# Kernel optimization log

Measured on AMD Instinct MI355X. Metric: run time of the kernel, lower is better.

The kernel has to match this reference:

```python
import math
import jax, jax.numpy as jnp
import numpy as np
from jax import lax

B, CIN, COUT, K, SDIM, H, W = 8, 64, 64, 3, 512, 256, 256
EPS = 1e-8

def setup_inputs() -> dict:
    key = jax.random.key(0)
    k1, k2, k3, k4 = jax.random.split(key, 4)
    return {
        "input": jax.random.normal(k1, (B, CIN, H, W), dtype=jnp.float32),
        "style": jax.random.normal(k2, (B, SDIM), dtype=jnp.float32),
        "weight": jax.random.normal(k3, (1, COUT, CIN, K, K), dtype=jnp.float32),
        "mod_weight": jax.random.normal(k4, (CIN, SDIM), dtype=jnp.float32),
        "mod_bias": jnp.ones((CIN,), dtype=jnp.float32),
    }

def reference(input, style, weight, mod_weight, mod_bias):
    b, cin, h, w = input.shape
    cout, k = weight.shape[1], weight.shape[3]
    scale = 1.0 / math.sqrt(cin * k * k)          # equalized-lr conv scale
    mod_scale = 1.0 / math.sqrt(mod_weight.shape[1])  # EqualLinear fan-in scale
    # style modulation: (B, Cin)
    s = jnp.einsum('bs,cs->bc', style, mod_weight) * mod_scale + mod_bias
    # modulated per-sample weights: (B, Cout, Cin, K, K)
    wmod = scale * weight * s[:, None, :, None, None]
    # demodulation over (Cin, K, K)
    demod = lax.rsqrt(jnp.sum(wmod * wmod, axis=(2, 3, 4)) + EPS)
    wmod = wmod * demod[:, :, None, None, None]
    # grouped conv with groups = batch
    x = input.reshape(1, b * cin, h, w)
    wg = wmod.reshape(b * cout, cin, k, k)
    pad = k // 2
    out = lax.conv_general_dilated(
        x, wg, window_strides=(1, 1), padding=[(pad, pad), (pad, pad)],
        dimension_numbers=('NCHW', 'OIHW', 'NCHW'), feature_group_count=b)
    return out.reshape(b, cout, h, w)
```

## Files before the change

### kernel.cpp

```cpp
#include <hip/hip_runtime.h>


#define CIN   64
#define COUT  64
#define SDIM  512
#define HW    256

typedef short bf16x8 __attribute__((ext_vector_type(8)));
typedef float f32x4  __attribute__((ext_vector_type(4)));
typedef unsigned short u16;

static __device__ __forceinline__ u16 f2bf(float f) {
    union { float f; unsigned u; } v; v.f = f;
    unsigned r = v.u + 0x7FFF + ((v.u >> 16) & 1);
    return (u16)(r >> 16);
}

__global__ void k_style(const float* __restrict__ style, const float* __restrict__ mw,
                        const float* __restrict__ mb, float* __restrict__ s_out) {
    int b = blockIdx.x;
    int t = threadIdx.x;
    int cin = t & 63, seg = t >> 6;
    const float4* st = (const float4*)(style + (size_t)b * SDIM) + seg * 32;
    const float4* w  = (const float4*)(mw + (size_t)cin * SDIM) + seg * 32;
    float acc = 0.f;
#pragma unroll 8
    for (int i = 0; i < 32; i++) {
        float4 a = st[i], bb = w[i];
        acc += a.x * bb.x + a.y * bb.y + a.z * bb.z + a.w * bb.w;
    }
    __shared__ float red[4][64];
    red[seg][cin] = acc;
    __syncthreads();
    if (seg == 0) {
        float v = red[0][cin] + red[1][cin] + red[2][cin] + red[3][cin];
        s_out[b * CIN + cin] = v * 0.04419417382415922f + mb[cin];
    }
}

__global__ void k_wdemod(const float* __restrict__ weight, const float* __restrict__ s,
                         u16* __restrict__ wA) {
    int bid = blockIdx.x;
    int b = bid >> 6, co = bid & 63;
    int cin = threadIdx.x;
    float sv = s[b * CIN + cin] * (1.0f / 24.0f);
    const float* wp = weight + ((size_t)co * CIN + cin) * 9;
    float w[9]; float sq = 0.f;
#pragma unroll
    for (int k = 0; k < 9; k++) { w[k] = wp[k] * sv; sq += w[k] * w[k]; }
#pragma unroll
    for (int off = 32; off; off >>= 1) sq += __shfl_xor(sq, off, 64);
    float dm = 1.0f / sqrtf(sq + 1e-8f);
    u16* dst = wA + (((size_t)b * COUT + co) * 9) * 64 + cin;
#pragma unroll
    for (int k = 0; k < 9; k++) dst[k * 64] = f2bf(w[k] * dm);
}

__global__ void k_transpose(const float* __restrict__ in, u16* __restrict__ X) {
    int bid = blockIdx.x;
    int wblk = bid & 3, h = (bid >> 2) & 255, b = bid >> 10;
    int w0 = wblk * 64;
    __shared__ u16 lds[64][65];
    int t = threadIdx.x;
    const float* src = in + (size_t)b * CIN * 65536 + (size_t)h * 256 + w0;
    int dw = t & 63, c0 = t >> 6;
#pragma unroll
    for (int i = 0; i < 16; i++) {
        int cin = i * 4 + c0;
        lds[cin][dw] = f2bf(src[(size_t)cin * 65536 + dw]);
    }
    __syncthreads();
    u16* dst = X + (((size_t)b * 256 + h) * 256 + w0) * 64;
#pragma unroll
    for (int i = 0; i < 4; i++) {
        int u = i * 256 + t;
        int dw2 = u >> 4, c4 = (u & 15) * 4;
        ushort4 val;
        val.x = lds[c4 + 0][dw2]; val.y = lds[c4 + 1][dw2];
        val.z = lds[c4 + 2][dw2]; val.w = lds[c4 + 3][dw2];
        *(ushort4*)(dst + (size_t)dw2 * 64 + c4) = val;
    }
}

__global__ __launch_bounds__(256, 2) void k_conv(
        const u16* __restrict__ X, const u16* __restrict__ wA,
        float* __restrict__ out) {
    int bid = blockIdx.x;
    int b = bid >> 8, r = bid & 255;
    int y0 = (r >> 2) << 2;
    int x0 = (r & 3) << 6;
    int wv = threadIdx.x >> 6;
    int l  = threadIdx.x & 63;
    int lr = l & 15, lg = l >> 4;
    int y = y0 + wv;

    f32x4 acc[4][4];
#pragma unroll
    for (int ct = 0; ct < 4; ct++)
#pragma unroll
        for (int xt = 0; xt < 4; xt++) acc[ct][xt] = (f32x4){0.f, 0.f, 0.f, 0.f};

    const u16* Xb  = X  + (size_t)b * 65536 * 64;
    const u16* wAb = wA + (size_t)b * COUT * 9 * 64;

#pragma unroll
    for (int kk = 0; kk < 9; kk++) {
        const int dh = kk / 3, dw = kk % 3;
        int yy = y + dh - 1;
        if (yy < 0 || yy > 255) continue;
        const u16* Xrow = Xb + (size_t)yy * 256 * 64;
#pragma unroll
        for (int half = 0; half < 2; half++) {
            bf16x8 afr[4], bfr[4];
#pragma unroll
            for (int ct = 0; ct < 4; ct++) {
                afr[ct] = *(const bf16x8*)(wAb + (((size_t)(ct * 16 + lr)) * 9 + kk) * 64
                                           + half * 32 + lg * 8);
            }
#pragma unroll
            for (int xt = 0; xt < 4; xt++) {
                int xx = x0 + xt * 16 + lr + dw - 1;
                bf16x8 v = {0, 0, 0, 0, 0, 0, 0, 0};
                if (xx >= 0 && xx < 256)
                    v = *(const bf16x8*)(Xrow + (size_t)xx * 64 + half * 32 + lg * 8);
                bfr[xt] = v;
            }
#pragma unroll
            for (int ct = 0; ct < 4; ct++)
#pragma unroll
                for (int xt = 0; xt < 4; xt++)
                    acc[ct][xt] = __builtin_amdgcn_mfma_f32_16x16x32_bf16(
                        afr[ct], bfr[xt], acc[ct][xt], 0, 0, 0);
        }
    }

    float* ob = out + (size_t)b * COUT * 65536 + (size_t)y * 256 + x0;
#pragma unroll
    for (int ct = 0; ct < 4; ct++)
#pragma unroll
        for (int xt = 0; xt < 4; xt++)
#pragma unroll
            for (int q = 0; q < 4; q++) {
                int cout = ct * 16 + lg * 4 + q;
                ob[(size_t)cout * 65536 + xt * 16 + lr] = acc[ct][xt][q];
            }
}

extern "C" void kernel_launch(void* const* d_in, const int* in_sizes, int n_in,
                              void* d_out, int out_size, void* d_ws, size_t ws_size,
                              hipStream_t stream) {
    const float* input      = (const float*)d_in[0];
    const float* style      = (const float*)d_in[1];
    const float* weight     = (const float*)d_in[2];
    const float* mod_weight = (const float*)d_in[3];
    const float* mod_bias   = (const float*)d_in[4];
    float* out = (float*)d_out;

    char* ws = (char*)d_ws;
    u16*   X  = (u16*)ws;
    u16*   wA = (u16*)(ws + 67108864);
    float* s  = (float*)(ws + 67108864 + 589824);

    k_style    <<<8,    256, 0, stream>>>(style, mod_weight, mod_bias, s);
    k_wdemod   <<<512,  64,  0, stream>>>(weight, s, wA);
    k_transpose<<<8192, 256, 0, stream>>>(input, X);
    k_conv     <<<2048, 256, 0, stream>>>(X, wA, out);
}
```

Before: 373.7 us.

## Fuse input transpose into conv via LDS halo tile and stage output stores

Removes the separate transpose kernel and its 64 MB bf16 intermediate. The conv kernel now loads an fp32 6x72x64 halo tile straight from the NCHW input, converts it to bf16 into XOR-swizzled LDS, and reads MFMA B fragments from LDS instead of global memory. The epilogue goes through LDS so each cout row is written with coalesced float4 stores, and block indices are swizzled across batches. In exchange, each block reloads halo rows that neighbouring blocks also read, and the kernel uses about 55 KB of LDS, which may limit occupancy.

```diff
diff --git a/kernel.cpp b/kernel.cpp
--- a/kernel.cpp
+++ b/kernel.cpp
@@ -1,19 +1,23 @@
 #include <hip/hip_runtime.h>
+#include <hip/hip_bf16.h>
 
 
 #define CIN   64
 #define COUT  64
 #define SDIM  512
-#define HW    256
 
 typedef short bf16x8 __attribute__((ext_vector_type(8)));
 typedef float f32x4  __attribute__((ext_vector_type(4)));
 typedef unsigned short u16;
+typedef unsigned short us8 __attribute__((ext_vector_type(8)));
 
 static __device__ __forceinline__ u16 f2bf(float f) {
     union { float f; unsigned u; } v; v.f = f;
     unsigned r = v.u + 0x7FFF + ((v.u >> 16) & 1);
     return (u16)(r >> 16);
+}
+static __device__ __forceinline__ float getc(const float4& f, int k) {
+    return k == 0 ? f.x : k == 1 ? f.y : k == 2 ? f.z : f.w;
 }
 
 __global__ void k_style(const float* __restrict__ style, const float* __restrict__ mw,
@@ -56,43 +60,53 @@
     for (int k = 0; k < 9; k++) dst[k * 64] = f2bf(w[k] * dm);
 }
 
-__global__ void k_transpose(const float* __restrict__ in, u16* __restrict__ X) {
-    int bid = blockIdx.x;
-    int wblk = bid & 3, h = (bid >> 2) & 255, b = bid >> 10;
-    int w0 = wblk * 64;
-    __shared__ u16 lds[64][65];
-    int t = threadIdx.x;
-    const float* src = in + (size_t)b * CIN * 65536 + (size_t)h * 256 + w0;
-    int dw = t & 63, c0 = t >> 6;
+__global__ __launch_bounds__(256, 2) void k_conv2(
+        const float* __restrict__ in, const u16* __restrict__ wA,
+        float* __restrict__ out) {
+    __shared__ __align__(16) u16 Xs[6 * 72 * 64];
+
+    int raw = blockIdx.x;
+    int swz = (raw & 7) * 256 + (raw >> 3);
+    int b = swz >> 8, r = swz & 255;
+    int y0 = (r >> 2) * 4, x0 = (r & 3) * 64;
+    int tid = threadIdx.x;
+
+    const float* inb = in + (size_t)b * (CIN * 65536);
+    for (int u = tid; u < 864; u += 256) {
+        int cing = u & 7;
+        int g = u >> 3;
+        int x4 = g % 18, yy = g / 18;
+        int y = y0 + yy - 1;
+        int x = x0 - 4 + x4 * 4;
+        float4 f[8];
+        if (y >= 0 && y < 256 && x >= 0 && x < 253) {
+            const float* p = inb + (size_t)(cing * 8) * 65536 + (size_t)y * 256 + x;
 #pragma unroll
-    for (int i = 0; i < 16; i++) {
-        int cin = i * 4 + c0;
-        lds[cin][dw] = f2bf(src[(size_t)cin * 65536 + dw]);
+            for (int j = 0; j < 8; j++) f[j] = *(const float4*)(p + (size_t)j * 65536);
+        } else {
+#pragma unroll
+            for (int j = 0; j < 8; j++) f[j] = make_float4(0.f, 0.f, 0.f, 0.f);
+        }
+#pragma unroll
+        for (int k = 0; k < 4; k++) {
+            union { us8 v; unsigned w[4]; } pk;
+#pragma unroll
+            for (int p2 = 0; p2 < 4; p2++) {
+                __hip_bfloat162 h = __float22bfloat162_rn(
+                    make_float2(getc(f[2 * p2], k), getc(f[2 * p2 + 1], k)));
+                unsigned wv_; __builtin_memcpy(&wv_, &h, 4);
+                pk.w[p2] = wv_;
+            }
+            int xl = x4 * 4 + k;
+            unsigned bo = (unsigned)(((yy * 72 + xl) * 64 + cing * 8) * 2)
+                        ^ ((unsigned)(xl & 7) << 4);
+            *(us8*)((char*)Xs + bo) = pk.v;
+        }
     }
     __syncthreads();
-    u16* dst = X + (((size_t)b * 256 + h) * 256 + w0) * 64;
-#pragma unroll
-    for (int i = 0; i < 4; i++) {
-        int u = i * 256 + t;
-        int dw2 = u >> 4, c4 = (u & 15) * 4;
-        ushort4 val;
-        val.x = lds[c4 + 0][dw2]; val.y = lds[c4 + 1][dw2];
-        val.z = lds[c4 + 2][dw2]; val.w = lds[c4 + 3][dw2];
-        *(ushort4*)(dst + (size_t)dw2 * 64 + c4) = val;
-    }
-}
 
-__global__ __launch_bounds__(256, 2) void k_conv(
-        const u16* __restrict__ X, const u16* __restrict__ wA,
-        float* __restrict__ out) {
-    int bid = blockIdx.x;
-    int b = bid >> 8, r = bid & 255;
-    int y0 = (r >> 2) << 2;
-    int x0 = (r & 3) << 6;
-    int wv = threadIdx.x >> 6;
-    int l  = threadIdx.x & 63;
-    int lr = l & 15, lg = l >> 4;
-    int y = y0 + wv;
+    int wv = tid >> 6, l = tid & 63, lr = l & 15, lg = l >> 4;
+    const u16* wAb = wA + (size_t)b * (COUT * 9 * 64);
 
     f32x4 acc[4][4];
 #pragma unroll
@@ -100,30 +114,23 @@
 #pragma unroll
         for (int xt = 0; xt < 4; xt++) acc[ct][xt] = (f32x4){0.f, 0.f, 0.f, 0.f};
 
-    const u16* Xb  = X  + (size_t)b * 65536 * 64;
-    const u16* wAb = wA + (size_t)b * COUT * 9 * 64;
-
 #pragma unroll
     for (int kk = 0; kk < 9; kk++) {
         const int dh = kk / 3, dw = kk % 3;
-        int yy = y + dh - 1;
-        if (yy < 0 || yy > 255) continue;
-        const u16* Xrow = Xb + (size_t)yy * 256 * 64;
+        const int yl = wv + dh;
 #pragma unroll
         for (int half = 0; half < 2; half++) {
             bf16x8 afr[4], bfr[4];
 #pragma unroll
-            for (int ct = 0; ct < 4; ct++) {
-                afr[ct] = *(const bf16x8*)(wAb + (((size_t)(ct * 16 + lr)) * 9 + kk) * 64
+            for (int ct = 0; ct < 4; ct++)
+                afr[ct] = *(const bf16x8*)(wAb + ((size_t)(ct * 16 + lr) * 9 + kk) * 64
                                            + half * 32 + lg * 8);
-            }
 #pragma unroll
             for (int xt = 0; xt < 4; xt++) {
-                int xx = x0 + xt * 16 + lr + dw - 1;
-                bf16x8 v = {0, 0, 0, 0, 0, 0, 0, 0};
-                if (xx >= 0 && xx < 256)
-                    v = *(const bf16x8*)(Xrow + (size_t)xx * 64 + half * 32 + lg * 8);
-                bfr[xt] = v;
+                int xl = xt * 16 + lr + dw + 3;
+                unsigned bo = (unsigned)(((yl * 72 + xl) * 64 + half * 32 + lg * 8) * 2)
+                            ^ ((unsigned)(xl & 7) << 4);
+                bfr[xt] = *(const bf16x8*)((const char*)Xs + bo);
             }
 #pragma unroll
             for (int ct = 0; ct < 4; ct++)
@@ -134,16 +141,24 @@
         }
     }
 
-    float* ob = out + (size_t)b * COUT * 65536 + (size_t)y * 256 + x0;
+    __syncthreads();
+    float* ep = ((float*)Xs) + wv * (16 * 68);
+    float* ob = out + ((size_t)b * COUT) * 65536 + (size_t)(y0 + wv) * 256 + x0;
+    int c = l >> 2, xq = l & 3;
 #pragma unroll
-    for (int ct = 0; ct < 4; ct++)
+    for (int ct = 0; ct < 4; ct++) {
 #pragma unroll
         for (int xt = 0; xt < 4; xt++)
 #pragma unroll
-            for (int q = 0; q < 4; q++) {
-                int cout = ct * 16 + lg * 4 + q;
-                ob[(size_t)cout * 65536 + xt * 16 + lr] = acc[ct][xt][q];
-            }
+            for (int q = 0; q < 4; q++)
+                ep[(lg * 4 + q) * 68 + xt * 16 + lr] = acc[ct][xt][q];
+        asm volatile("s_waitcnt lgkmcnt(0)" ::: "memory");
+#pragma unroll
+        for (int k = 0; k < 4; k++) {
+            float4 v = *(const float4*)(ep + c * 68 + k * 16 + xq * 4);
+            *(float4*)(ob + (size_t)(ct * 16 + c) * 65536 + k * 16 + xq * 4) = v;
+        }
+    }
 }
 
 extern "C" void kernel_launch(void* const* d_in, const int* in_sizes, int n_in,
@@ -157,12 +172,10 @@
     float* out = (float*)d_out;
 
     char* ws = (char*)d_ws;
-    u16*   X  = (u16*)ws;
-    u16*   wA = (u16*)(ws + 67108864);
-    float* s  = (float*)(ws + 67108864 + 589824);
+    u16*   wA = (u16*)ws;
+    float* s  = (float*)(ws + 589824);
 
-    k_style    <<<8,    256, 0, stream>>>(style, mod_weight, mod_bias, s);
-    k_wdemod   <<<512,  64,  0, stream>>>(weight, s, wA);
-    k_transpose<<<8192, 256, 0, stream>>>(input, X);
-    k_conv     <<<2048, 256, 0, stream>>>(X, wA, out);
+    k_style <<<8,    256, 0, stream>>>(style, mod_weight, mod_bias, s);
+    k_wdemod<<<512,  64,  0, stream>>>(weight, s, wA);
+    k_conv2 <<<2048, 256, 0, stream>>>(input, wA, out);
 }
```

Result: faster. 324.4 us (-13.2%).
